# Optimization experiments

Hardware: AMD Instinct MI355X
Metric: run time of the kernel (lower is better)

The kernel has to match this reference:

```python
import jax, jax.numpy as jnp
import numpy as np

N_PER, B, DEG = 1000, 20, 32
N = N_PER * B            # 20000 nodes
D_IN, D_OUT = 128, 128
K_PER = 50
ASSIGN = K_PER * B       # 1000 clusters total (block-diagonal per graph)
E = N_PER * DEG * B      # 640000 edges


def setup_inputs() -> dict:
    key = jax.random.key(0)
    k1, k2, k3, k4 = jax.random.split(key, 4)
    h = jax.random.normal(k1, (N, D_IN), dtype=jnp.float32)
    W_feat = jax.random.normal(k2, (2 * D_IN, D_OUT), dtype=jnp.float32) * 0.05
    b_feat = jnp.zeros((D_OUT,), jnp.float32)
    W_pool = jax.random.normal(k3, (2 * D_IN, ASSIGN), dtype=jnp.float32) * 0.05
    b_pool = jnp.zeros((ASSIGN,), jnp.float32)
    # block-structured edges: each graph's edges stay within its node range
    e = jax.random.randint(k4, (B, N_PER * DEG, 2), 0, N_PER)
    e = e + (jnp.arange(B) * N_PER)[:, None, None]
    e = e.reshape(-1, 2)
    src = e[:, 0].astype(jnp.int32)
    dst = e[:, 1].astype(jnp.int32)
    # block-diagonal assignment mask (scipy.linalg.block_diag of ones blocks)
    gid_node = jnp.repeat(jnp.arange(B), N_PER)   # graph id of each node
    gid_col = jnp.repeat(jnp.arange(B), K_PER)    # graph id of each cluster col
    mask = (gid_node[:, None] == gid_col[None, :]).astype(jnp.float32)
    return dict(h=h, W_feat=W_feat, b_feat=b_feat, W_pool=W_pool,
                b_pool=b_pool, src=src, dst=dst, mask=mask)


def _graphsage(h, src, dst, W, b):
    # mean aggregator over incoming edges: c[d] = mean_{(s,d) in E} h[s]
    msum = jax.ops.segment_sum(h[src], dst, num_segments=N)
    cnt = jax.ops.segment_sum(jnp.ones((src.shape[0], 1), h.dtype), dst,
                              num_segments=N)
    c = msum / jnp.maximum(cnt, 1.0)
    # Bundler: Linear(cat(h, c)) -> L2 normalize -> activation
    z = jnp.concatenate([h, c], axis=1) @ W + b
    z = z / jnp.maximum(jnp.linalg.norm(z, axis=1, keepdims=True), 1e-12)
    return jax.nn.relu(z)


def reference(h, W_feat, b_feat, W_pool, b_pool, src, dst, mask):
    feat = _graphsage(h, src, dst, W_feat, b_feat)        # [N, D_OUT]
    assign = _graphsage(h, src, dst, W_pool, b_pool)      # [N, ASSIGN]
    # masked_softmax (memory_efficient=False, allennlp-style)
    p = jax.nn.softmax(assign * mask, axis=-1)
    p = p * mask
    p = p / (jnp.sum(p, axis=-1, keepdims=True) + 1e-13)  # [N, ASSIGN]
    h_pool = p.T @ feat                                   # [ASSIGN, D_OUT]
    # sparse A @ S, with A[dst, src] = 1 per edge (DGL adjacency convention)
    a_s = jax.ops.segment_sum(p[src], dst, num_segments=N)  # [N, ASSIGN]
    adj_new = p.T @ a_s                                     # [ASSIGN, ASSIGN]
    return adj_new, h_pool
```

## Files before the change

kernel.cpp:

```cpp
#include <hip/hip_runtime.h>

#define NN 20000
#define NPG 1000
#define NBG 20
#define DD 128
#define KK2 256
#define KPC 50
#define KPAD 64
#define NAC 1000
#define NACP 1024
#define NPGP 1024
#define NNT 20480
#define NEDGE 640000
#define CAP 96
#define OUTSZ 1128000

typedef __attribute__((ext_vector_type(8))) short bfrag;
typedef __attribute__((ext_vector_type(4))) float f32x4;
typedef __attribute__((ext_vector_type(8))) unsigned short ushort8;
typedef __attribute__((ext_vector_type(8))) _Float16 half8;

__device__ __forceinline__ unsigned short f2bf(float f) {
  unsigned int u = __builtin_bit_cast(unsigned int, f);
  unsigned int r = (u + 0x7FFFu + ((u >> 16) & 1u)) >> 16;
  return (unsigned short)r;
}
__device__ __forceinline__ float bf2f(unsigned short u) {
  return __builtin_bit_cast(float, ((unsigned int)u) << 16);
}

__device__ __forceinline__ int xcd_swz(int orig, int nwg) {
  int q = nwg >> 3, r = nwg & 7;
  int x = orig & 7, idx = orig >> 3;
  return (x < r) ? (x * (q + 1) + idx) : (r * (q + 1) + (x - r) * q + idx);
}

__global__ __launch_bounds__(256) void k_zero(int* __restrict__ deg) {
  int idx = blockIdx.x * 256 + threadIdx.x;
  if (idx < 5000) ((int4*)deg)[idx] = make_int4(0, 0, 0, 0);
}

__global__ __launch_bounds__(256) void k_prep(
    const float* __restrict__ h, const float* __restrict__ Wf,
    const float* __restrict__ Wp, const float* __restrict__ bp,
    const int* __restrict__ src, const int* __restrict__ dst,
    int* __restrict__ deg, int* __restrict__ ssrc,
    unsigned short* __restrict__ xb,
    unsigned short* __restrict__ Wtp, unsigned short* __restrict__ Wtf,
    unsigned short* __restrict__ Wpb,
    float* __restrict__ v, float* __restrict__ bb,
    unsigned short* __restrict__ pT, float* __restrict__ out) {
  __shared__ float red[256];
  int b = blockIdx.x;
  int tid = threadIdx.x;
  if (b < 2500) {
    int e = b * 256 + tid;
    if (e < NEDGE) {
      int d = dst[e];
      int pos = atomicAdd(&deg[d], 1);
      ssrc[d * CAP + pos] = src[e];
    }
  } else if (b < 3750) {
    int idx = (b - 2500) * 256 + tid;
    int n = idx >> 4, seg = idx & 15;
    const float4* hp = (const float4*)(h + n * DD + seg * 8);
    float4 x0 = hp[0], x1 = hp[1];
    ushort8 o;
    o[0] = f2bf(x0.x); o[1] = f2bf(x0.y); o[2] = f2bf(x0.z); o[3] = f2bf(x0.w);
    o[4] = f2bf(x1.x); o[5] = f2bf(x1.y); o[6] = f2bf(x1.z); o[7] = f2bf(x1.w);
    *(ushort8*)(xb + n * KK2 + seg * 8) = o;
  } else if (b < 4006) {
    int wid = tid >> 6, lane = tid & 63;
    int col = (b - 3750) * 4 + wid;
    #pragma unroll
    for (int i = 0; i < 4; ++i) {
      int kk = i * 64 + lane;
      float val = (col < NAC) ? Wp[kk * NAC + col] : 0.f;
      Wtp[col * KK2 + kk] = f2bf(val);
    }
  } else if (b < 4038) {
    int wid = tid >> 6, lane = tid & 63;
    int col = (b - 4006) * 4 + wid;
    #pragma unroll
    for (int i = 0; i < 4; ++i) {
      int kk = i * 64 + lane;
      Wtf[col * KK2 + kk] = f2bf(Wf[kk * DD + col]);
    }
  } else if (b < 4166) {
    int idx = (b - 4038) * 256 + tid;
    int rrow = idx >> 7;
    int seg = idx & 127;
    ushort8 o;
    #pragma unroll
    for (int i = 0; i < 8; ++i) {
      int cc = seg * 8 + i;
      o[i] = (cc < NAC) ? f2bf(Wp[rrow * NAC + cc]) : (unsigned short)0;
    }
    *(ushort8*)(Wpb + rrow * NACP + seg * 8) = o;
  } else if (b < 4422) {
    int i = b - 4166;
    float acc = 0.f;
    for (int k = tid; k < NAC; k += 256) acc += Wp[i * NAC + k] * bp[k];
    red[tid] = acc;
    __syncthreads();
    for (int st = 128; st > 0; st >>= 1) {
      if (tid < st) red[tid] += red[tid + st];
      __syncthreads();
    }
    if (tid == 0) v[i] = red[0];
    if (i == 0) {
      __syncthreads();
      float a2 = 0.f;
      for (int k = tid; k < NAC; k += 256) { float t = bp[k]; a2 += t * t; }
      red[tid] = a2;
      __syncthreads();
      for (int st = 128; st > 0; st >>= 1) {
        if (tid < st) red[tid] += red[tid + st];
        __syncthreads();
      }
      if (tid == 0) *bb = red[0];
    }
  } else if (b < 5062) {
    int idx = (b - 4422) * 256 + tid;
    ((int4*)pT)[idx] = make_int4(0, 0, 0, 0);
  } else {
    int idx = (b - 5062) * 256 + tid;
    if (idx < OUTSZ / 4) ((float4*)out)[idx] = make_float4(0.f, 0.f, 0.f, 0.f);
  }
}

__global__ __launch_bounds__(256) void k_mid(
    const unsigned short* __restrict__ Wpb, unsigned short* __restrict__ Gb,
    const int* __restrict__ deg, const int* __restrict__ ssrc,
    unsigned short* __restrict__ xb) {
  int b = blockIdx.x;
  int tid = threadIdx.x;
  if (b < 16) {
    int i0 = (b & 3) * 64, j0 = (b >> 2) * 64;
    int wid = tid >> 6, lane = tid & 63;
    int lr = lane & 15, lg = lane >> 4;
    f32x4 acc[4] = {};
    for (int kt = 0; kt < 32; ++kt) {
      bfrag a[4], bfr;
      #pragma unroll
      for (int m = 0; m < 4; ++m)
        a[m] = *reinterpret_cast<const bfrag*>(Wpb + (size_t)(i0 + m * 16 + lr) * NACP + kt * 32 + lg * 8);
      bfr = *reinterpret_cast<const bfrag*>(Wpb + (size_t)(j0 + wid * 16 + lr) * NACP + kt * 32 + lg * 8);
      #pragma unroll
      for (int m = 0; m < 4; ++m)
        acc[m] = __builtin_amdgcn_mfma_f32_16x16x32_bf16(a[m], bfr, acc[m], 0, 0, 0);
    }
    #pragma unroll
    for (int m = 0; m < 4; ++m)
      #pragma unroll
      for (int r = 0; r < 4; ++r) {
        int row = i0 + m * 16 + lg * 4 + r;
        int col = j0 + wid * 16 + lr;
        Gb[row * 256 + col] = f2bf(acc[m][r]);
      }
  } else {
    int wg = xcd_swz(b - 16, 1250);
    int node = wg * 16 + (tid >> 4);
    int lane = tid & 15;
    int dg = deg[node];
    const int* sl = ssrc + node * CAP;
    float a[8] = {};
    int j = 0;
    for (; j + 8 <= dg; j += 8) {
      int4 ia = *(const int4*)&sl[j];
      int4 ib = *(const int4*)&sl[j + 4];
      ushort8 w0 = *(const ushort8*)(xb + (size_t)ia.x * KK2 + lane * 8);
      ushort8 w1 = *(const ushort8*)(xb + (size_t)ia.y * KK2 + lane * 8);
      ushort8 w2 = *(const ushort8*)(xb + (size_t)ia.z * KK2 + lane * 8);
      ushort8 w3 = *(const ushort8*)(xb + (size_t)ia.w * KK2 + lane * 8);
      ushort8 w4 = *(const ushort8*)(xb + (size_t)ib.x * KK2 + lane * 8);
      ushort8 w5 = *(const ushort8*)(xb + (size_t)ib.y * KK2 + lane * 8);
      ushort8 w6 = *(const ushort8*)(xb + (size_t)ib.z * KK2 + lane * 8);
      ushort8 w7 = *(const ushort8*)(xb + (size_t)ib.w * KK2 + lane * 8);
      #pragma unroll
      for (int i = 0; i < 8; ++i)
        a[i] += ((bf2f(w0[i]) + bf2f(w1[i])) + (bf2f(w2[i]) + bf2f(w3[i]))) +
                ((bf2f(w4[i]) + bf2f(w5[i])) + (bf2f(w6[i]) + bf2f(w7[i])));
    }
    for (; j + 4 <= dg; j += 4) {
      int4 idx = *(const int4*)&sl[j];
      ushort8 v0 = *(const ushort8*)(xb + (size_t)idx.x * KK2 + lane * 8);
      ushort8 v1 = *(const ushort8*)(xb + (size_t)idx.y * KK2 + lane * 8);
      ushort8 v2 = *(const ushort8*)(xb + (size_t)idx.z * KK2 + lane * 8);
      ushort8 v3 = *(const ushort8*)(xb + (size_t)idx.w * KK2 + lane * 8);
      #pragma unroll
      for (int i = 0; i < 8; ++i)
        a[i] += bf2f(v0[i]) + bf2f(v1[i]) + bf2f(v2[i]) + bf2f(v3[i]);
    }
    for (; j < dg; ++j) {
      ushort8 vv = *(const ushort8*)(xb + (size_t)sl[j] * KK2 + lane * 8);
      #pragma unroll
      for (int i = 0; i < 8; ++i) a[i] += bf2f(vv[i]);
    }
    float inv = 1.f / (float)max(dg, 1);
    ushort8 o;
    #pragma unroll
    for (int i = 0; i < 8; ++i) o[i] = f2bf(a[i] * inv);
    *(ushort8*)(xb + node * KK2 + DD + lane * 8) = o;
  }
}

__global__ __launch_bounds__(256) void k_fused(
    const unsigned short* __restrict__ xb, const unsigned short* __restrict__ Gb,
    const unsigned short* __restrict__ Wtp, const unsigned short* __restrict__ Wtf,
    const float* __restrict__ bp, const float* __restrict__ bfeat,
    const float* __restrict__ v, const float* __restrict__ bbp,
    unsigned short* __restrict__ featT, _Float16* __restrict__ p_pad,
    unsigned short* __restrict__ pT) {
  __shared__ int4 xs4[1024];
  __shared__ float zbuf[32][52];
  __shared__ float nrm_lds[32];
  __shared__ float nrmf_lds[32];
  int n0 = blockIdx.x * 32;
  int tid = threadIdx.x;
  for (int i = tid; i < 1024; i += 256) {
    int row = i >> 5;
    xs4[i ^ (row & 7)] = ((const int4*)xb)[(size_t)(n0 + row) * 32 + (i & 31)];
  }
  if (tid < 32) { nrm_lds[tid] = 0.f; nrmf_lds[tid] = 0.f; }
  __syncthreads();

  int wid = tid >> 6, lane = tid & 63;
  int lr = lane & 15, lg = lane >> 4;
  const unsigned short* xsu = (const unsigned short*)xs4;

  {
    f32x4 accy[2][4] = {};
    #pragma unroll
    for (int kt = 0; kt < 8; ++kt) {
      bfrag a[2], bfr[4];
      #pragma unroll
      for (int m = 0; m < 2; ++m) {
        int slot = (m * 16 + lr) * 32 + kt * 4 + lg;
        a[m] = *reinterpret_cast<const bfrag*>(&xs4[slot ^ ((slot >> 5) & 7)]);
      }
      #pragma unroll
      for (int c = 0; c < 4; ++c) {
        int j = wid * 64 + c * 16 + lr;
        bfr[c] = *reinterpret_cast<const bfrag*>(Gb + (size_t)j * KK2 + kt * 32 + lg * 8);
      }
      #pragma unroll
      for (int m = 0; m < 2; ++m)
        #pragma unroll
        for (int c = 0; c < 4; ++c)
          accy[m][c] = __builtin_amdgcn_mfma_f32_16x16x32_bf16(a[m], bfr[c], accy[m][c], 0, 0, 0);
    }
    float vv[4];
    #pragma unroll
    for (int c = 0; c < 4; ++c) vv[c] = v[wid * 64 + c * 16 + lr];
    #pragma unroll
    for (int m = 0; m < 2; ++m)
      #pragma unroll
      for (int r = 0; r < 4; ++r) {
        int row = m * 16 + lg * 4 + r;
        float part = 0.f;
        #pragma unroll
        for (int c = 0; c < 4; ++c) {
          int k = wid * 64 + c * 16 + lr;
          int slot = row * 32 + (k >> 3);
          float xv = bf2f(xsu[(size_t)(slot ^ (row & 7)) * 8 + (k & 7)]);
          part += (accy[m][c][r] + 2.f * vv[c]) * xv;
        }
        part += __shfl_xor(part, 1); part += __shfl_xor(part, 2);
        part += __shfl_xor(part, 4); part += __shfl_xor(part, 8);
        if (lr == 0) atomicAdd(&nrm_lds[row], part);
      }
  }

  {
    int g0 = n0 / NPG;
    int g1 = (n0 + 31) / NPG;
    for (int gp = g0; gp <= g1; ++gp) {
      int wb = gp * KPC;
      f32x4 accw[2] = {};
      #pragma unroll
      for (int kt = 0; kt < 8; ++kt) {
        bfrag a[2], bfr;
        #pragma unroll
        for (int m = 0; m < 2; ++m) {
          int slot = (m * 16 + lr) * 32 + kt * 4 + lg;
          a[m] = *reinterpret_cast<const bfrag*>(&xs4[slot ^ ((slot >> 5) & 7)]);
        }
        bfr = *reinterpret_cast<const bfrag*>(Wtp + (size_t)(wb + wid * 16 + lr) * KK2 + kt * 32 + lg * 8);
        #pragma unroll
        for (int m = 0; m < 2; ++m)
          accw[m] = __builtin_amdgcn_mfma_f32_16x16x32_bf16(a[m], bfr, accw[m], 0, 0, 0);
      }
      int wc = wid * 16 + lr;
      float bias = (wc < KPC) ? bp[wb + wc] : 0.f;
      #pragma unroll
      for (int m = 0; m < 2; ++m)
        #pragma unroll
        for (int r = 0; r < 4; ++r) {
          int row = m * 16 + lg * 4 + r;
          if (wc < KPC && (n0 + row) / NPG == gp)
            zbuf[row][wc] = accw[m][r] + bias;
        }
    }
  }

  f32x4 accf[2][2] = {};
  {
    #pragma unroll
    for (int kt = 0; kt < 8; ++kt) {
      bfrag a[2], bfr[2];
      #pragma unroll
      for (int m = 0; m < 2; ++m) {
        int slot = (m * 16 + lr) * 32 + kt * 4 + lg;
        a[m] = *reinterpret_cast<const bfrag*>(&xs4[slot ^ ((slot >> 5) & 7)]);
      }
      #pragma unroll
      for (int c = 0; c < 2; ++c) {
        int col = wid * 32 + c * 16 + lr;
        bfr[c] = *reinterpret_cast<const bfrag*>(Wtf + (size_t)col * KK2 + kt * 32 + lg * 8);
      }
      #pragma unroll
      for (int m = 0; m < 2; ++m)
        #pragma unroll
        for (int c = 0; c < 2; ++c)
          accf[m][c] = __builtin_amdgcn_mfma_f32_16x16x32_bf16(a[m], bfr[c], accf[m][c], 0, 0, 0);
    }
    float nf[2][4] = {};
    #pragma unroll
    for (int c = 0; c < 2; ++c) {
      int col = wid * 32 + c * 16 + lr;
      float bias = bfeat[col];
      #pragma unroll
      for (int m = 0; m < 2; ++m)
        #pragma unroll
        for (int r = 0; r < 4; ++r) {
          float z = accf[m][c][r] + bias;
          accf[m][c][r] = z;
          nf[m][r] += z * z;
        }
    }
    #pragma unroll
    for (int m = 0; m < 2; ++m)
      #pragma unroll
      for (int r = 0; r < 4; ++r) {
        float p = nf[m][r];
        p += __shfl_xor(p, 1); p += __shfl_xor(p, 2);
        p += __shfl_xor(p, 4); p += __shfl_xor(p, 8);
        if (lr == 0) atomicAdd(&nrmf_lds[m * 16 + lg * 4 + r], p);
      }
  }
  __syncthreads();

  unsigned short* ftl = (unsigned short*)xs4;
  #pragma unroll
  for (int m = 0; m < 2; ++m)
    #pragma unroll
    for (int r = 0; r < 4; ++r) {
      int row = m * 16 + lg * 4 + r;
      float sc = 1.f / fmaxf(sqrtf(nrmf_lds[row]), 1e-12f);
      #pragma unroll
      for (int c = 0; c < 2; ++c) {
        int col = wid * 32 + c * 16 + lr;
        ftl[col * 40 + row] = f2bf(fmaxf(accf[m][c][r] * sc, 0.f));
      }
    }

  if (tid < 128) {
    int node = tid >> 2, q = tid & 3;
    float nv = nrm_lds[node] + bbp[0];
    float inv = 1.f / fmaxf(sqrtf(fmaxf(nv, 0.f)), 1e-12f);
    float e[16];
    float mx = -1e30f;
    #pragma unroll
    for (int i = 0; i < 16; ++i) {
      int cc = q * 16 + i;
      float sv = (cc < KPC) ? fmaxf(zbuf[node][cc] * inv, 0.f) : -1e30f;
      e[i] = sv;
      mx = fmaxf(mx, sv);
    }
    mx = fmaxf(mx, __shfl_xor(mx, 1));
    mx = fmaxf(mx, __shfl_xor(mx, 2));
    float esum = 0.f;
    #pragma unroll
    for (int i = 0; i < 16; ++i) {
      int cc = q * 16 + i;
      float ev = (cc < KPC) ? __expf(e[i] - mx) : 0.f;
      e[i] = ev;
      esum += ev;
    }
    esum += __shfl_xor(esum, 1);
    esum += __shfl_xor(esum, 2);
    float isum = 1.f / esum;
    int n = n0 + node;
    int gg = n / NPG;
    int nloc = n - gg * NPG;
    half8 o0, o1;
    #pragma unroll
    for (int i = 0; i < 8; ++i) {
      o0[i] = (_Float16)(e[i] * isum);
      o1[i] = (_Float16)(e[i + 8] * isum);
    }
    *(half8*)&p_pad[(size_t)n * KPAD + q * 16] = o0;
    *(half8*)&p_pad[(size_t)n * KPAD + q * 16 + 8] = o1;
    #pragma unroll
    for (int i = 0; i < 16; ++i) {
      int cc = q * 16 + i;
      pT[((size_t)gg * KPAD + cc) * NPGP + nloc] = f2bf(e[i] * isum);
    }
  }
  __syncthreads();

  #pragma unroll
  for (int pass = 0; pass < 2; ++pass) {
    int ch = tid + pass * 256;
    int col = ch >> 2, off = (ch & 3) * 8;
    *(ushort8*)(featT + (size_t)col * NNT + n0 + off) = *(const ushort8*)&ftl[col * 40 + off];
  }
}

__global__ __launch_bounds__(256) void k_as(
    const _Float16* __restrict__ p_pad, const int* __restrict__ deg,
    const int* __restrict__ ssrc, unsigned short* __restrict__ asT) {
  __shared__ unsigned short as_lds[64 * 40];
  int tid = threadIdx.x;
  int wg = xcd_swz(blockIdx.x, 625);
  int nrow = tid >> 3;
  int n = wg * 32 + nrow;
  int lane = tid & 7;
  int dg = deg[n];
  const int* sl = ssrc + n * CAP;
  float a[8] = {};
  int j = 0;
  for (; j + 8 <= dg; j += 8) {
    int4 ia = *(const int4*)&sl[j];
    int4 ib = *(const int4*)&sl[j + 4];
    half8 w0 = *(const half8*)(p_pad + (size_t)ia.x * KPAD + lane * 8);
    half8 w1 = *(const half8*)(p_pad + (size_t)ia.y * KPAD + lane * 8);
    half8 w2 = *(const half8*)(p_pad + (size_t)ia.z * KPAD + lane * 8);
    half8 w3 = *(const half8*)(p_pad + (size_t)ia.w * KPAD + lane * 8);
    half8 w4 = *(const half8*)(p_pad + (size_t)ib.x * KPAD + lane * 8);
    half8 w5 = *(const half8*)(p_pad + (size_t)ib.y * KPAD + lane * 8);
    half8 w6 = *(const half8*)(p_pad + (size_t)ib.z * KPAD + lane * 8);
    half8 w7 = *(const half8*)(p_pad + (size_t)ib.w * KPAD + lane * 8);
    #pragma unroll
    for (int i = 0; i < 8; ++i)
      a[i] += (((float)w0[i] + (float)w1[i]) + ((float)w2[i] + (float)w3[i])) +
              (((float)w4[i] + (float)w5[i]) + ((float)w6[i] + (float)w7[i]));
  }
  for (; j + 4 <= dg; j += 4) {
    int4 idx = *(const int4*)&sl[j];
    half8 v0 = *(const half8*)(p_pad + (size_t)idx.x * KPAD + lane * 8);
    half8 v1 = *(const half8*)(p_pad + (size_t)idx.y * KPAD + lane * 8);
    half8 v2 = *(const half8*)(p_pad + (size_t)idx.z * KPAD + lane * 8);
    half8 v3 = *(const half8*)(p_pad + (size_t)idx.w * KPAD + lane * 8);
    #pragma unroll
    for (int i = 0; i < 8; ++i)
      a[i] += (float)v0[i] + (float)v1[i] + (float)v2[i] + (float)v3[i];
  }
  for (; j < dg; ++j) {
    half8 vv = *(const half8*)(p_pad + (size_t)sl[j] * KPAD + lane * 8);
    #pragma unroll
    for (int i = 0; i < 8; ++i) a[i] += (float)vv[i];
  }
  #pragma unroll
  for (int i = 0; i < 8; ++i)
    as_lds[(lane * 8 + i) * 40 + nrow] = f2bf(a[i]);
  __syncthreads();
  {
    int col = tid >> 2, off = (tid & 3) * 8;
    *(ushort8*)(asT + (size_t)col * NNT + wg * 32 + off) = *(const ushort8*)&as_lds[col * 40 + off];
  }
}

__global__ __launch_bounds__(256) void k_final(
    const unsigned short* __restrict__ pT, const unsigned short* __restrict__ featT,
    const unsigned short* __restrict__ asT, float* __restrict__ out) {
  int g = blockIdx.x >> 3;
  int kc = blockIdx.x & 7;
  int tid = threadIdx.x;
  int wid = tid >> 6, lane = tid & 63;
  int lr = lane & 15, lg = lane >> 4;
  f32x4 acc[3][4] = {};
  const unsigned short* bbase[3];
  #pragma unroll
  for (int j = 0; j < 3; ++j) {
    int cf = wid * 3 + j;
    bbase[j] = (cf < 8) ? (featT + (size_t)(cf * 16 + lr) * NNT)
                        : (asT + (size_t)((cf - 8) * 16 + lr) * NNT);
  }
  int nb0 = g * NPG + kc * 128;
  #pragma unroll
  for (int ks = 0; ks < 4; ++ks) {
    bfrag a[4], bfr[3];
    #pragma unroll
    for (int m = 0; m < 4; ++m)
      a[m] = *(const bfrag*)(pT + ((size_t)g * KPAD + m * 16 + lr) * NPGP + kc * 128 + ks * 32 + lg * 8);
    #pragma unroll
    for (int j = 0; j < 3; ++j)
      bfr[j] = *(const bfrag*)(bbase[j] + nb0 + ks * 32 + lg * 8);
    #pragma unroll
    for (int j = 0; j < 3; ++j)
      #pragma unroll
      for (int m = 0; m < 4; ++m)
        acc[j][m] = __builtin_amdgcn_mfma_f32_16x16x32_bf16(a[m], bfr[j], acc[j][m], 0, 0, 0);
  }
  #pragma unroll
  for (int j = 0; j < 3; ++j) {
    int cf = wid * 3 + j;
    #pragma unroll
    for (int m = 0; m < 4; ++m)
      #pragma unroll
      for (int r = 0; r < 4; ++r) {
        int i = m * 16 + lg * 4 + r;
        if (i < KPC) {
          if (cf < 8) {
            int col = cf * 16 + lr;
            atomicAdd(&out[1000000 + (size_t)(g * KPC + i) * DD + col], acc[j][m][r]);
          } else {
            int col2 = (cf - 8) * 16 + lr;
            if (col2 < KPC)
              atomicAdd(&out[(size_t)(g * KPC + i) * NAC + g * KPC + col2], acc[j][m][r]);
          }
        }
      }
  }
}

extern "C" void kernel_launch(void* const* d_in, const int* in_sizes, int n_in,
                              void* d_out, int out_size, void* d_ws, size_t ws_size,
                              hipStream_t stream) {
  const float* h = (const float*)d_in[0];
  const float* Wf = (const float*)d_in[1];
  const float* bf = (const float*)d_in[2];
  const float* Wp = (const float*)d_in[3];
  const float* bp = (const float*)d_in[4];
  const int* src = (const int*)d_in[5];
  const int* dst = (const int*)d_in[6];
  float* out = (float*)d_out;
  char* ws = (char*)d_ws;

  int* deg = (int*)(ws + 0);
  int* ssrc = (int*)(ws + 80000);
  unsigned short* xb = (unsigned short*)(ws + 7760000);
  _Float16* p_pad = (_Float16*)(ws + 18000000);
  unsigned short* featT = (unsigned short*)(ws + 20560000);
  unsigned short* asT = (unsigned short*)(ws + 25802880);
  unsigned short* Wpb = (unsigned short*)(ws + 28424320);
  unsigned short* Gb = (unsigned short*)(ws + 28948608);
  float* v = (float*)(ws + 29079680);
  float* bb = (float*)(ws + 29080704);
  unsigned short* Wtp = (unsigned short*)(ws + 29081728);
  unsigned short* Wtf = (unsigned short*)(ws + 29606016);
  unsigned short* pT = (unsigned short*)(ws + 29671552);

  k_zero<<<20, 256, 0, stream>>>(deg);
  k_prep<<<6164, 256, 0, stream>>>(h, Wf, Wp, bp, src, dst, deg, ssrc, xb, Wtp, Wtf, Wpb, v, bb, pT, out);
  k_mid<<<1266, 256, 0, stream>>>(Wpb, Gb, deg, ssrc, xb);
  k_fused<<<625, 256, 0, stream>>>(xb, Gb, Wtp, Wtf, bp, bf, v, bb, featT, p_pad, pT);
  k_as<<<625, 256, 0, stream>>>(p_pad, deg, ssrc, asT);
  k_final<<<160, 256, 0, stream>>>(pT, featT, asT, out);
}
```

Before: 117.8 us.

## Move feature GEMM from k_fused into extra blocks of the k_as gather kernel

The feature-branch linear layer, its L2 normalization and the featT transpose store move out of k_fused into 313 additional blocks appended to k_as, using 64-node tiles instead of 32. This shortens k_fused's critical path and lets the compute-bound feature GEMM run alongside the memory-bound p_pad gather, balancing the two kernels. It raises k_as's LDS use to 32KB for all blocks, which may lower occupancy for the gather blocks.

```diff
diff --git a/kernel.cpp b/kernel.cpp
--- a/kernel.cpp
+++ b/kernel.cpp
@@ -207,22 +207,20 @@
 
 __global__ __launch_bounds__(256) void k_fused(
     const unsigned short* __restrict__ xb, const unsigned short* __restrict__ Gb,
-    const unsigned short* __restrict__ Wtp, const unsigned short* __restrict__ Wtf,
-    const float* __restrict__ bp, const float* __restrict__ bfeat,
+    const unsigned short* __restrict__ Wtp,
+    const float* __restrict__ bp,
     const float* __restrict__ v, const float* __restrict__ bbp,
-    unsigned short* __restrict__ featT, _Float16* __restrict__ p_pad,
-    unsigned short* __restrict__ pT) {
+    _Float16* __restrict__ p_pad, unsigned short* __restrict__ pT) {
   __shared__ int4 xs4[1024];
   __shared__ float zbuf[32][52];
   __shared__ float nrm_lds[32];
-  __shared__ float nrmf_lds[32];
   int n0 = blockIdx.x * 32;
   int tid = threadIdx.x;
   for (int i = tid; i < 1024; i += 256) {
     int row = i >> 5;
     xs4[i ^ (row & 7)] = ((const int4*)xb)[(size_t)(n0 + row) * 32 + (i & 31)];
   }
-  if (tid < 32) { nrm_lds[tid] = 0.f; nrmf_lds[tid] = 0.f; }
+  if (tid < 32) nrm_lds[tid] = 0.f;
   __syncthreads();
 
   int wid = tid >> 6, lane = tid & 63;
@@ -303,67 +301,7 @@
         }
     }
   }
-
-  f32x4 accf[2][2] = {};
-  {
-    #pragma unroll
-    for (int kt = 0; kt < 8; ++kt) {
-      bfrag a[2], bfr[2];
-      #pragma unroll
-      for (int m = 0; m < 2; ++m) {
-        int slot = (m * 16 + lr) * 32 + kt * 4 + lg;
-        a[m] = *reinterpret_cast<const bfrag*>(&xs4[slot ^ ((slot >> 5) & 7)]);
-      }
-      #pragma unroll
-      for (int c = 0; c < 2; ++c) {
-        int col = wid * 32 + c * 16 + lr;
-        bfr[c] = *reinterpret_cast<const bfrag*>(Wtf + (size_t)col * KK2 + kt * 32 + lg * 8);
-      }
-      #pragma unroll
-      for (int m = 0; m < 2; ++m)
-        #pragma unroll
-        for (int c = 0; c < 2; ++c)
-          accf[m][c] = __builtin_amdgcn_mfma_f32_16x16x32_bf16(a[m], bfr[c], accf[m][c], 0, 0, 0);
-    }
-    float nf[2][4] = {};
-    #pragma unroll
-    for (int c = 0; c < 2; ++c) {
-      int col = wid * 32 + c * 16 + lr;
-      float bias = bfeat[col];
-      #pragma unroll
-      for (int m = 0; m < 2; ++m)
-        #pragma unroll
-        for (int r = 0; r < 4; ++r) {
-          float z = accf[m][c][r] + bias;
-          accf[m][c][r] = z;
-          nf[m][r] += z * z;
-        }
-    }
-    #pragma unroll
-    for (int m = 0; m < 2; ++m)
-      #pragma unroll
-      for (int r = 0; r < 4; ++r) {
-        float p = nf[m][r];
-        p += __shfl_xor(p, 1); p += __shfl_xor(p, 2);
-        p += __shfl_xor(p, 4); p += __shfl_xor(p, 8);
-        if (lr == 0) atomicAdd(&nrmf_lds[m * 16 + lg * 4 + r], p);
-      }
-  }
   __syncthreads();
-
-  unsigned short* ftl = (unsigned short*)xs4;
-  #pragma unroll
-  for (int m = 0; m < 2; ++m)
-    #pragma unroll
-    for (int r = 0; r < 4; ++r) {
-      int row = m * 16 + lg * 4 + r;
-      float sc = 1.f / fmaxf(sqrtf(nrmf_lds[row]), 1e-12f);
-      #pragma unroll
-      for (int c = 0; c < 2; ++c) {
-        int col = wid * 32 + c * 16 + lr;
-        ftl[col * 40 + row] = f2bf(fmaxf(accf[m][c][r] * sc, 0.f));
-      }
-    }
 
   if (tid < 128) {
     int node = tid >> 2, q = tid & 3;
@@ -408,67 +346,144 @@
       pT[((size_t)gg * KPAD + cc) * NPGP + nloc] = f2bf(e[i] * isum);
     }
   }
-  __syncthreads();
-
-  #pragma unroll
-  for (int pass = 0; pass < 2; ++pass) {
-    int ch = tid + pass * 256;
-    int col = ch >> 2, off = (ch & 3) * 8;
-    *(ushort8*)(featT + (size_t)col * NNT + n0 + off) = *(const ushort8*)&ftl[col * 40 + off];
-  }
 }
 
 __global__ __launch_bounds__(256) void k_as(
     const _Float16* __restrict__ p_pad, const int* __restrict__ deg,
-    const int* __restrict__ ssrc, unsigned short* __restrict__ asT) {
-  __shared__ unsigned short as_lds[64 * 40];
+    const int* __restrict__ ssrc, unsigned short* __restrict__ asT,
+    const unsigned short* __restrict__ xb, const unsigned short* __restrict__ Wtf,
+    const float* __restrict__ bfeat, unsigned short* __restrict__ featT) {
+  __shared__ int4 big[2048];
+  __shared__ float nrmf[64];
+  int b = blockIdx.x;
   int tid = threadIdx.x;
-  int wg = xcd_swz(blockIdx.x, 625);
-  int nrow = tid >> 3;
-  int n = wg * 32 + nrow;
-  int lane = tid & 7;
-  int dg = deg[n];
-  const int* sl = ssrc + n * CAP;
-  float a[8] = {};
-  int j = 0;
-  for (; j + 8 <= dg; j += 8) {
-    int4 ia = *(const int4*)&sl[j];
-    int4 ib = *(const int4*)&sl[j + 4];
-    half8 w0 = *(const half8*)(p_pad + (size_t)ia.x * KPAD + lane * 8);
-    half8 w1 = *(const half8*)(p_pad + (size_t)ia.y * KPAD + lane * 8);
-    half8 w2 = *(const half8*)(p_pad + (size_t)ia.z * KPAD + lane * 8);
-    half8 w3 = *(const half8*)(p_pad + (size_t)ia.w * KPAD + lane * 8);
-    half8 w4 = *(const half8*)(p_pad + (size_t)ib.x * KPAD + lane * 8);
-    half8 w5 = *(const half8*)(p_pad + (size_t)ib.y * KPAD + lane * 8);
-    half8 w6 = *(const half8*)(p_pad + (size_t)ib.z * KPAD + lane * 8);
-    half8 w7 = *(const half8*)(p_pad + (size_t)ib.w * KPAD + lane * 8);
+  if (b < 625) {
+    unsigned short* as_lds = (unsigned short*)big;
+    int wg = xcd_swz(b, 625);
+    int nrow = tid >> 3;
+    int n = wg * 32 + nrow;
+    int lane = tid & 7;
+    int dg = deg[n];
+    const int* sl = ssrc + n * CAP;
+    float a[8] = {};
+    int j = 0;
+    for (; j + 8 <= dg; j += 8) {
+      int4 ia = *(const int4*)&sl[j];
+      int4 ib = *(const int4*)&sl[j + 4];
+      half8 w0 = *(const half8*)(p_pad + (size_t)ia.x * KPAD + lane * 8);
+      half8 w1 = *(const half8*)(p_pad + (size_t)ia.y * KPAD + lane * 8);
+      half8 w2 = *(const half8*)(p_pad + (size_t)ia.z * KPAD + lane * 8);
+      half8 w3 = *(const half8*)(p_pad + (size_t)ia.w * KPAD + lane * 8);
+      half8 w4 = *(const half8*)(p_pad + (size_t)ib.x * KPAD + lane * 8);
+      half8 w5 = *(const half8*)(p_pad + (size_t)ib.y * KPAD + lane * 8);
+      half8 w6 = *(const half8*)(p_pad + (size_t)ib.z * KPAD + lane * 8);
+      half8 w7 = *(const half8*)(p_pad + (size_t)ib.w * KPAD + lane * 8);
+      #pragma unroll
+      for (int i = 0; i < 8; ++i)
+        a[i] += (((float)w0[i] + (float)w1[i]) + ((float)w2[i] + (float)w3[i])) +
+                (((float)w4[i] + (float)w5[i]) + ((float)w6[i] + (float)w7[i]));
+    }
+    for (; j + 4 <= dg; j += 4) {
+      int4 idx = *(const int4*)&sl[j];
+      half8 v0 = *(const half8*)(p_pad + (size_t)idx.x * KPAD + lane * 8);
+      half8 v1 = *(const half8*)(p_pad + (size_t)idx.y * KPAD + lane * 8);
+      half8 v2 = *(const half8*)(p_pad + (size_t)idx.z * KPAD + lane * 8);
+      half8 v3 = *(const half8*)(p_pad + (size_t)idx.w * KPAD + lane * 8);
+      #pragma unroll
+      for (int i = 0; i < 8; ++i)
+        a[i] += (float)v0[i] + (float)v1[i] + (float)v2[i] + (float)v3[i];
+    }
+    for (; j < dg; ++j) {
+      half8 vv = *(const half8*)(p_pad + (size_t)sl[j] * KPAD + lane * 8);
+      #pragma unroll
+      for (int i = 0; i < 8; ++i) a[i] += (float)vv[i];
+    }
     #pragma unroll
     for (int i = 0; i < 8; ++i)
-      a[i] += (((float)w0[i] + (float)w1[i]) + ((float)w2[i] + (float)w3[i])) +
-              (((float)w4[i] + (float)w5[i]) + ((float)w6[i] + (float)w7[i]));
-  }
-  for (; j + 4 <= dg; j += 4) {
-    int4 idx = *(const int4*)&sl[j];
-    half8 v0 = *(const half8*)(p_pad + (size_t)idx.x * KPAD + lane * 8);
-    half8 v1 = *(const half8*)(p_pad + (size_t)idx.y * KPAD + lane * 8);
-    half8 v2 = *(const half8*)(p_pad + (size_t)idx.z * KPAD + lane * 8);
-    half8 v3 = *(const half8*)(p_pad + (size_t)idx.w * KPAD + lane * 8);
-    #pragma unroll
-    for (int i = 0; i < 8; ++i)
-      a[i] += (float)v0[i] + (float)v1[i] + (float)v2[i] + (float)v3[i];
-  }
-  for (; j < dg; ++j) {
-    half8 vv = *(const half8*)(p_pad + (size_t)sl[j] * KPAD + lane * 8);
-    #pragma unroll
-    for (int i = 0; i < 8; ++i) a[i] += (float)vv[i];
-  }
-  #pragma unroll
-  for (int i = 0; i < 8; ++i)
-    as_lds[(lane * 8 + i) * 40 + nrow] = f2bf(a[i]);
-  __syncthreads();
-  {
-    int col = tid >> 2, off = (tid & 3) * 8;
-    *(ushort8*)(asT + (size_t)col * NNT + wg * 32 + off) = *(const ushort8*)&as_lds[col * 40 + off];
+      as_lds[(lane * 8 + i) * 40 + nrow] = f2bf(a[i]);
+    __syncthreads();
+    {
+      int col = tid >> 2, off = (tid & 3) * 8;
+      *(ushort8*)(asT + (size_t)col * NNT + wg * 32 + off) = *(const ushort8*)&as_lds[col * 40 + off];
+    }
+  } else {
+    int n0 = (b - 625) * 64;
+    int nt = min(64, NN - n0);
+    for (int i = tid; i < 2048; i += 256) {
+      int row = i >> 5;
+      int4 vv = make_int4(0, 0, 0, 0);
+      if (row < nt) vv = ((const int4*)xb)[(size_t)(n0 + row) * 32 + (i & 31)];
+      big[i ^ (row & 7)] = vv;
+    }
+    if (tid < 64) nrmf[tid] = 0.f;
+    __syncthreads();
+    int wid = tid >> 6, lane = tid & 63;
+    int lr = lane & 15, lg = lane >> 4;
+    f32x4 acc[4][2] = {};
+    #pragma unroll
+    for (int kt = 0; kt < 8; ++kt) {
+      bfrag a[4], bfr[2];
+      #pragma unroll
+      for (int m = 0; m < 4; ++m) {
+        int slot = (m * 16 + lr) * 32 + kt * 4 + lg;
+        a[m] = *reinterpret_cast<const bfrag*>(&big[slot ^ ((slot >> 5) & 7)]);
+      }
+      #pragma unroll
+      for (int c = 0; c < 2; ++c) {
+        int col = wid * 32 + c * 16 + lr;
+        bfr[c] = *reinterpret_cast<const bfrag*>(Wtf + (size_t)col * KK2 + kt * 32 + lg * 8);
+      }
+      #pragma unroll
+      for (int m = 0; m < 4; ++m)
+        #pragma unroll
+        for (int c = 0; c < 2; ++c)
+          acc[m][c] = __builtin_amdgcn_mfma_f32_16x16x32_bf16(a[m], bfr[c], acc[m][c], 0, 0, 0);
+    }
+    float nf[4][4] = {};
+    #pragma unroll
+    for (int c = 0; c < 2; ++c) {
+      int col = wid * 32 + c * 16 + lr;
+      float bias = bfeat[col];
+      #pragma unroll
+      for (int m = 0; m < 4; ++m)
+        #pragma unroll
+        for (int r = 0; r < 4; ++r) {
+          float z = acc[m][c][r] + bias;
+          acc[m][c][r] = z;
+          nf[m][r] += z * z;
+        }
+    }
+    #pragma unroll
+    for (int m = 0; m < 4; ++m)
+      #pragma unroll
+      for (int r = 0; r < 4; ++r) {
+        float p = nf[m][r];
+        p += __shfl_xor(p, 1); p += __shfl_xor(p, 2);
+        p += __shfl_xor(p, 4); p += __shfl_xor(p, 8);
+        if (lr == 0) atomicAdd(&nrmf[m * 16 + lg * 4 + r], p);
+      }
+    __syncthreads();
+    unsigned short* ftl = (unsigned short*)big;
+    #pragma unroll
+    for (int m = 0; m < 4; ++m)
+      #pragma unroll
+      for (int r = 0; r < 4; ++r) {
+        int row = m * 16 + lg * 4 + r;
+        float sc = 1.f / fmaxf(sqrtf(nrmf[row]), 1e-12f);
+        #pragma unroll
+        for (int c = 0; c < 2; ++c) {
+          int col = wid * 32 + c * 16 + lr;
+          ftl[col * 72 + row] = f2bf(fmaxf(acc[m][c][r] * sc, 0.f));
+        }
+      }
+    __syncthreads();
+    #pragma unroll
+    for (int p2 = 0; p2 < 4; ++p2) {
+      int c2 = tid + p2 * 256;
+      int col = c2 >> 3, off = (c2 & 7) * 8;
+      if (n0 + off < NN)
+        *(ushort8*)(featT + (size_t)col * NNT + n0 + off) = *(const ushort8*)&ftl[col * 72 + off];
+    }
   }
 }
 
@@ -556,7 +571,7 @@
   k_zero<<<20, 256, 0, stream>>>(deg);
   k_prep<<<6164, 256, 0, stream>>>(h, Wf, Wp, bp, src, dst, deg, ssrc, xb, Wtp, Wtf, Wpb, v, bb, pT, out);
   k_mid<<<1266, 256, 0, stream>>>(Wpb, Gb, deg, ssrc, xb);
-  k_fused<<<625, 256, 0, stream>>>(xb, Gb, Wtp, Wtf, bp, bf, v, bb, featT, p_pad, pT);
-  k_as<<<625, 256, 0, stream>>>(p_pad, deg, ssrc, asT);
+  k_fused<<<625, 256, 0, stream>>>(xb, Gb, Wtp, bp, v, bb, p_pad, pT);
+  k_as<<<938, 256, 0, stream>>>(p_pad, deg, ssrc, asT, xb, Wtf, bf, featT);
   k_final<<<160, 256, 0, stream>>>(pT, featT, asT, out);
 }
```

After: 121.0 us. +2.7%, slower.
